# Optimization experiments

Measured on AMD Instinct MI355X. Metric: run time of the kernel, lower is better.

## Reference

```python
import jax, jax.numpy as jnp
import numpy as np

B, R, L, F, H = 65536, 12, 16, 8, 64  # batch, rss_dim, n_leds, led_feat_dim, head_dim

def setup_inputs() -> dict:
    key = jax.random.key(0)
    ks = jax.random.split(key, 20)
    p = lambda k, shp, s=0.1: (jax.random.normal(k, shp, dtype=jnp.float32) * s)
    return {
        "rss_t": jax.random.uniform(ks[0], (B, R, 1), dtype=jnp.float32),
        "led_features": jax.random.normal(ks[1], (B, L, F), dtype=jnp.float32),
        "led_positions": jax.random.normal(ks[2], (B, L, 3), dtype=jnp.float32),
        "prev_pos": jax.random.normal(ks[3], (B, 3), dtype=jnp.float32),
        "freq_mask": jax.random.randint(ks[4], (R, L), 0, 2).astype(jnp.int32),
        # intensity_gate: Linear(1,16) -> ReLU -> Linear(16,1) -> Sigmoid
        "gw1": p(ks[5], (1, 16)), "gb1": p(ks[6], (16,)),
        "gw2": p(ks[7], (16, 1)), "gb2": p(ks[8], (1,)),
        # query_proj: Linear(1,32) -> ReLU -> Linear(32,64)
        "qw1": p(ks[9], (1, 32)), "qb1": p(ks[10], (32,)),
        "qw2": p(ks[11], (32, H)), "qb2": p(ks[12], (H,)),
        # key_proj: Linear(F+3,32) -> ReLU -> Linear(32,64)
        "kw1": p(ks[13], (F + 3, 32)), "kb1": p(ks[14], (32,)),
        "kw2": p(ks[15], (32, H)), "kb2": p(ks[16], (H,)),
        "sigma": jnp.float32(0.5),
    }

def reference(rss_t, led_features, led_positions, prev_pos, freq_mask,
              gw1, gb1, gw2, gb2, qw1, qb1, qw2, qb2, kw1, kb1, kw2, kb2, sigma):
    # intensity gate with hard threshold
    gate = jax.nn.sigmoid(jax.nn.relu(rss_t @ gw1 + gb1) @ gw2 + gb2)  # [B,R,1]
    iw = (rss_t > 0.5).astype(rss_t.dtype) * gate                      # [B,R,1]
    # query / key projections
    Q = jax.nn.relu((rss_t * iw) @ qw1 + qb1) @ qw2 + qb2              # [B,R,H]
    led_input = jnp.concatenate([led_features, led_positions], axis=-1)  # [B,L,F+3]
    K = jax.nn.relu(led_input @ kw1 + kb1) @ kw2 + kb2                 # [B,L,H]
    scores = jnp.einsum("brh,blh->brl", Q, K)                          # [B,R,L]
    # distance bias
    dist_sq = jnp.sum((prev_pos[:, None, :] - led_positions) ** 2, axis=-1)  # [B,L]
    scores = scores - dist_sq[:, None, :] / (2.0 * sigma ** 2)
    # mask + softmax
    neg = jnp.finfo(scores.dtype).min
    scores = jnp.where(freq_mask[None, :, :] == 0, neg, scores)
    attn = jax.nn.softmax(scores, axis=-1)                             # [B,R,L]
    return attn, iw.squeeze(-1)
```

## Files before the change

### kernel.cpp

```cpp
#include <hip/hip_runtime.h>

#define B_TOT 65536
#define R 12
#define L 16
#define NB 16
#define NEG_MIN -3.402823466e38f

#define WS_V   0
#define WS_C   32
#define WS_PM  40
#define WS_BP  64
#define WS_TAB 96
#define TROW   72

typedef __attribute__((ext_vector_type(8))) short short8;
typedef __attribute__((ext_vector_type(4))) float f32x4;

static __device__ __forceinline__ short f2bf(float f) {
    uint32_t u = __float_as_uint(f);
    uint32_t r = u + 0x7FFFu + ((u >> 16) & 1u);
    return (short)(r >> 16);
}

__global__ __launch_bounds__(256) void nfh_pre(
    const float* __restrict__ qw1, const float* __restrict__ qb1,
    const float* __restrict__ qw2, const float* __restrict__ qb2,
    const float* __restrict__ kw2, const float* __restrict__ kb2,
    const int*   __restrict__ fmask,
    float* __restrict__ ws)
{
    __shared__ float sM[1024];
    __shared__ float su[32];
    __shared__ float sw1[32], sb1[32], sbp[32];
    const int t = threadIdx.x;

    if (t < 32) { sw1[t] = qw1[t]; sb1[t] = qb1[t]; }
    for (int e = t; e < 1024; e += 256) {
        const int i = e >> 5, j = e & 31;
        float acc = 0.f;
        for (int h = 0; h < 64; ++h) acc = fmaf(qw2[i * 64 + h], kw2[j * 64 + h], acc);
        sM[e] = acc;
    }
    if (t < 32) {
        float au = 0.f, av = 0.f;
        for (int h = 0; h < 64; ++h) {
            au = fmaf(qw2[t * 64 + h], kb2[h], au);
            av = fmaf(kw2[t * 64 + h], qb2[h], av);
        }
        su[t] = au;
        ws[WS_V + t] = av;
        const float w = qw1[t];
        sbp[t] = (w != 0.f) ? (-qb1[t] / w) : 3.0e30f;
    }
    if (t == 64) {
        float acc = 0.f;
        for (int h = 0; h < 64; ++h) acc = fmaf(qb2[h], kb2[h], acc);
        ws[WS_C] = acc;
    }
    if (t < 12) {
        int pm = 0;
        for (int l = 0; l < 16; ++l) if (fmask[t * 16 + l] != 0) pm |= (1 << l);
        ((int*)ws)[WS_PM + t] = pm;
    }
    __syncthreads();
    if (t == 0) {
        for (int i = 1; i < 32; ++i) {
            float key = sbp[i]; int j = i - 1;
            while (j >= 0 && sbp[j] > key) { sbp[j + 1] = sbp[j]; --j; }
            sbp[j + 1] = key;
        }
    }
    __syncthreads();
    if (t < 32) ws[WS_BP + t] = sbp[t];

    for (int task = t; task < 33 * 32 + 33; task += 256) {
        const int m = (task < 33 * 32) ? (task >> 5) : (task - 33 * 32);
        const float xi = (m == 0) ? sbp[0] - 1.f
                       : ((m == 32) ? sbp[31] + 1.f
                                    : sbp[m - 1] + 0.5f * (sbp[m] - sbp[m - 1]));
        if (task < 33 * 32) {
            const int j = task & 31;
            float A = 0.f, Bv = 0.f;
            for (int i = 0; i < 32; ++i) {
                if (fmaf(sw1[i], xi, sb1[i]) > 0.f) {
                    A  = fmaf(sw1[i], sM[i * 32 + j], A);
                    Bv = fmaf(sb1[i], sM[i * 32 + j], Bv);
                }
            }
            ws[WS_TAB + m * TROW + j] = A;
            ws[WS_TAB + m * TROW + 36 + j] = Bv;
        } else {
            float Au = 0.f, Bu = 0.f;
            for (int i = 0; i < 32; ++i) {
                if (fmaf(sw1[i], xi, sb1[i]) > 0.f) {
                    Au = fmaf(sw1[i], su[i], Au);
                    Bu = fmaf(sb1[i], su[i], Bu);
                }
            }
            ws[WS_TAB + m * TROW + 32] = Au;
            ws[WS_TAB + m * TROW + 36 + 32] = Bu;
        }
    }
}

__global__ __launch_bounds__(256) void nfh_main(
    const float* __restrict__ rss,
    const float* __restrict__ feat,
    const float* __restrict__ pos,
    const float* __restrict__ prev,
    const float* __restrict__ gw1, const float* __restrict__ gb1,
    const float* __restrict__ gw2, const float* __restrict__ gb2,
    const float* __restrict__ kw1, const float* __restrict__ kb1,
    const float* __restrict__ sigma_p,
    const float* __restrict__ ws,
    float* __restrict__ out)
{
    __shared__ short s_bhf[NB * 512];
    __shared__ short s_ttf[NB * 512];
    __shared__ float s_vb[NB * 16];
    __shared__ float s_tc[NB * 16];
    __shared__ int   s_pm[16];

    const int t = threadIdx.x;
    const int b0 = blockIdx.x * NB;
    const float sigma = sigma_p[0];
    const float inv2s2 = 1.f / (2.f * sigma * sigma);

    if (t < 16) s_pm[t] = (t < 12) ? ((const int*)ws)[WS_PM + t] : 0;

    {
        const int bb1 = t >> 4, l1 = t & 15;
        const int b = b0 + bb1;
        float in[11];
        const float4* f4 = (const float4*)(feat + ((size_t)b * (L * 8) + l1 * 8));
        const float4 fa = f4[0], fb = f4[1];
        in[0] = fa.x; in[1] = fa.y; in[2] = fa.z; in[3] = fa.w;
        in[4] = fb.x; in[5] = fb.y; in[6] = fb.z; in[7] = fb.w;
        const float* pp = pos + ((size_t)b * (L * 3) + l1 * 3);
        in[8] = pp[0]; in[9] = pp[1]; in[10] = pp[2];

        float dsq = 0.f;
        #pragma unroll
        for (int m = 0; m < 3; ++m) {
            const float d = prev[b * 3 + m] - in[8 + m];
            dsq = fmaf(d, d, dsq);
        }
        float bh[32];
        #pragma unroll
        for (int j = 0; j < 32; ++j) bh[j] = kb1[j];
        #pragma unroll
        for (int m = 0; m < 11; ++m) {
            const float im = in[m];
            #pragma unroll
            for (int j = 0; j < 32; ++j) bh[j] = fmaf(im, kw1[m * 32 + j], bh[j]);
        }
        float vb = ws[WS_C];
        #pragma unroll
        for (int j = 0; j < 32; ++j) {
            bh[j] = fmaxf(bh[j], 0.f);
            vb = fmaf(ws[WS_V + j], bh[j], vb);
        }
        s_vb[bb1 * 16 + l1] = vb - dsq * inv2s2;

        #pragma unroll
        for (int kb = 0; kb < 4; ++kb) {
            short8 pk;
            #pragma unroll
            for (int j = 0; j < 8; ++j) pk[j] = f2bf(bh[kb * 8 + j]);
            *(short8*)&s_bhf[bb1 * 512 + (kb * 16 + l1) * 8] = pk;
        }
    }

    if (t < NB * R) {
        const int bb2 = t / R;
        const int r2 = t - bb2 * R;
        const float x = rss[(size_t)b0 * R + t];
        float z = gb2[0];
        #pragma unroll
        for (int i = 0; i < 16; ++i) {
            const float h = fmaxf(fmaf(x, gw1[i], gb1[i]), 0.f);
            z = fmaf(h, gw2[i], z);
        }
        const float gate = 1.f / (1.f + __expf(-z));
        const float iw = (x > 0.5f) ? gate : 0.f;
        out[(size_t)B_TOT * R * L + (size_t)b0 * R + t] = iw;
        const float xq = x * iw;

        int k = 0;
        #pragma unroll
        for (int m = 0; m < 32; ++m) k += (xq > ws[WS_BP + m]) ? 1 : 0;
        const float* row = ws + WS_TAB + k * TROW;
        const float4* ra = (const float4*)row;
        const float4* rb = (const float4*)(row + 36);
        s_tc[bb2 * 16 + r2] = fmaf(xq, row[32], row[68]);
        #pragma unroll
        for (int kb = 0; kb < 4; ++kb) {
            const float4 a0 = ra[kb * 2], b0_ = rb[kb * 2];
            const float4 a1 = ra[kb * 2 + 1], b1_ = rb[kb * 2 + 1];
            short8 pk;
            pk[0] = f2bf(fmaf(xq, a0.x, b0_.x));
            pk[1] = f2bf(fmaf(xq, a0.y, b0_.y));
            pk[2] = f2bf(fmaf(xq, a0.z, b0_.z));
            pk[3] = f2bf(fmaf(xq, a0.w, b0_.w));
            pk[4] = f2bf(fmaf(xq, a1.x, b1_.x));
            pk[5] = f2bf(fmaf(xq, a1.y, b1_.y));
            pk[6] = f2bf(fmaf(xq, a1.z, b1_.z));
            pk[7] = f2bf(fmaf(xq, a1.w, b1_.w));
            *(short8*)&s_ttf[bb2 * 512 + (kb * 16 + r2) * 8] = pk;
        }
    } else {
        const int u = t - 192;
        const int bb = u >> 2, r = 12 + (u & 3);
        const short8 z8 = {0, 0, 0, 0, 0, 0, 0, 0};
        #pragma unroll
        for (int kb = 0; kb < 4; ++kb)
            *(short8*)&s_ttf[bb * 512 + (kb * 16 + r) * 8] = z8;
        s_tc[bb * 16 + r] = 0.f;
    }
    __syncthreads();

    {
        const int lane = t & 63;
        const int w = t >> 6;
        const int r = lane & 15;
        const int lg = lane >> 4;
        const int pm = s_pm[r];

        #pragma unroll
        for (int i = 0; i < 4; ++i) {
            const int bb = w * 4 + i;
            const short8 af = *(const short8*)&s_bhf[bb * 512 + lane * 8];
            const short8 bf = *(const short8*)&s_ttf[bb * 512 + lane * 8];
            f32x4 acc = {0.f, 0.f, 0.f, 0.f};
            acc = __builtin_amdgcn_mfma_f32_16x16x32_bf16(af, bf, acc, 0, 0, 0);

            const float tc = s_tc[bb * 16 + r];
            const f32x4 vb4 = *(const f32x4*)&s_vb[bb * 16 + lg * 4];

            float sc[4];
            #pragma unroll
            for (int j = 0; j < 4; ++j) {
                sc[j] = acc[j] + tc + vb4[j];
                if (!((pm >> (lg * 4 + j)) & 1)) sc[j] = NEG_MIN;
            }
            float mx = fmaxf(fmaxf(sc[0], sc[1]), fmaxf(sc[2], sc[3]));
            mx = fmaxf(mx, __shfl_xor(mx, 16));
            mx = fmaxf(mx, __shfl_xor(mx, 32));
            float sum = 0.f;
            #pragma unroll
            for (int j = 0; j < 4; ++j) { sc[j] = __expf(sc[j] - mx); sum += sc[j]; }
            sum += __shfl_xor(sum, 16);
            sum += __shfl_xor(sum, 32);
            const float inv = 1.f / sum;

            if (r < R) {
                float4* op = (float4*)(out + ((size_t)(b0 + bb) * R + r) * L + lg * 4);
                *op = make_float4(sc[0] * inv, sc[1] * inv, sc[2] * inv, sc[3] * inv);
            }
        }
    }
}

extern "C" void kernel_launch(void* const* d_in, const int* in_sizes, int n_in,
                              void* d_out, int out_size, void* d_ws, size_t ws_size,
                              hipStream_t stream) {
    const float* rss   = (const float*)d_in[0];
    const float* feat  = (const float*)d_in[1];
    const float* pos   = (const float*)d_in[2];
    const float* prev  = (const float*)d_in[3];
    const int*   fmask = (const int*)d_in[4];
    const float* gw1   = (const float*)d_in[5];
    const float* gb1   = (const float*)d_in[6];
    const float* gw2   = (const float*)d_in[7];
    const float* gb2   = (const float*)d_in[8];
    const float* qw1   = (const float*)d_in[9];
    const float* qb1   = (const float*)d_in[10];
    const float* qw2   = (const float*)d_in[11];
    const float* qb2   = (const float*)d_in[12];
    const float* kw1   = (const float*)d_in[13];
    const float* kb1   = (const float*)d_in[14];
    const float* kw2   = (const float*)d_in[15];
    const float* kb2   = (const float*)d_in[16];
    const float* sigma = (const float*)d_in[17];
    float* out = (float*)d_out;
    float* ws  = (float*)d_ws;

    nfh_pre<<<1, 256, 0, stream>>>(qw1, qb1, qw2, qb2, kw2, kb2, fmask, ws);
    nfh_main<<<B_TOT / NB, 256, 0, stream>>>(
        rss, feat, pos, prev,
        gw1, gb1, gw2, gb2, kw1, kb1,
        sigma, ws, out);
}
```

Baseline: 181.6 us.

## Compute key hidden layer with bf16 MFMA and fold value bias into query table

Replaces the per-thread scalar FMA loop for the key MLP first layer with a 32x32x16 bf16 MFMA. The inputs are features, positions and a constant 1 for the bias, packed into LDS, and the packed kw1/kb1 weights are precomputed in the pre-kernel. The v·bh + c value-bias term is folded into the query lookup table, so the main kernel no longer computes it per LED. Block size drops to 8 batches and 128 threads, and LDS strides are padded, presumably to avoid bank conflicts. This trades heavy scalar ALU work for matrix-core work, but rounding inputs to bf16 before the first layer adds precision error.

```diff
diff --git a/kernel.cpp b/kernel.cpp
--- a/kernel.cpp
+++ b/kernel.cpp
@@ -3,7 +3,7 @@
 #define B_TOT 65536
 #define R 12
 #define L 16
-#define NB 16
+#define NB 8
 #define NEG_MIN -3.402823466e38f
 
 #define WS_V   0
@@ -12,26 +12,39 @@
 #define WS_BP  64
 #define WS_TAB 96
 #define TROW   72
-
-typedef __attribute__((ext_vector_type(8))) short short8;
-typedef __attribute__((ext_vector_type(4))) float f32x4;
+#define WS_KW  2472
+
+#define TTF_BSTR 520
+#define BHF_BSTR 576
+
+typedef __attribute__((ext_vector_type(8)))  short short8;
+typedef __attribute__((ext_vector_type(4)))  float f32x4;
+typedef __attribute__((ext_vector_type(16))) float f32x16;
 
 static __device__ __forceinline__ short f2bf(float f) {
     uint32_t u = __float_as_uint(f);
     uint32_t r = u + 0x7FFFu + ((u >> 16) & 1u);
     return (short)(r >> 16);
 }
+static __device__ __forceinline__ int pack2(float f0, float f1) {
+    uint32_t u0 = __float_as_uint(f0), u1 = __float_as_uint(f1);
+    uint32_t r0 = u0 + 0x7FFFu + ((u0 >> 16) & 1u);
+    uint32_t r1 = u1 + 0x7FFFu + ((u1 >> 16) & 1u);
+    return (int)((r0 >> 16) | (r1 & 0xFFFF0000u));
+}
 
 __global__ __launch_bounds__(256) void nfh_pre(
     const float* __restrict__ qw1, const float* __restrict__ qb1,
     const float* __restrict__ qw2, const float* __restrict__ qb2,
+    const float* __restrict__ kw1, const float* __restrict__ kb1,
     const float* __restrict__ kw2, const float* __restrict__ kb2,
     const int*   __restrict__ fmask,
     float* __restrict__ ws)
 {
     __shared__ float sM[1024];
-    __shared__ float su[32];
+    __shared__ float su[32], sv[32];
     __shared__ float sw1[32], sb1[32], sbp[32];
+    __shared__ float scc[1];
     const int t = threadIdx.x;
 
     if (t < 32) { sw1[t] = qw1[t]; sb1[t] = qb1[t]; }
@@ -48,6 +61,7 @@
             av = fmaf(kw2[t * 64 + h], qb2[h], av);
         }
         su[t] = au;
+        sv[t] = av;
         ws[WS_V + t] = av;
         const float w = qw1[t];
         sbp[t] = (w != 0.f) ? (-qb1[t] / w) : 3.0e30f;
@@ -56,11 +70,26 @@
         float acc = 0.f;
         for (int h = 0; h < 64; ++h) acc = fmaf(qb2[h], kb2[h], acc);
         ws[WS_C] = acc;
+        scc[0] = acc;
     }
     if (t < 12) {
         int pm = 0;
         for (int l = 0; l < 16; ++l) if (fmask[t * 16 + l] != 0) pm |= (1 << l);
         ((int*)ws)[WS_PM + t] = pm;
+    }
+    if (t < 64) {
+        const int j = t & 31;
+        int w4[4];
+        #pragma unroll
+        for (int q = 0; q < 4; ++q) {
+            float v0, v1;
+            const int k0 = (t >> 5) * 8 + q * 2, k1 = k0 + 1;
+            v0 = (k0 < 11) ? kw1[k0 * 32 + j] : ((k0 == 11) ? kb1[j] : 0.f);
+            v1 = (k1 < 11) ? kw1[k1 * 32 + j] : ((k1 == 11) ? kb1[j] : 0.f);
+            w4[q] = pack2(v0, v1);
+        }
+        int* wp = (int*)ws + WS_KW + t * 4;
+        wp[0] = w4[0]; wp[1] = w4[1]; wp[2] = w4[2]; wp[3] = w4[3];
     }
     __syncthreads();
     if (t == 0) {
@@ -88,7 +117,7 @@
                 }
             }
             ws[WS_TAB + m * TROW + j] = A;
-            ws[WS_TAB + m * TROW + 36 + j] = Bv;
+            ws[WS_TAB + m * TROW + 36 + j] = Bv + sv[j];
         } else {
             float Au = 0.f, Bu = 0.f;
             for (int i = 0; i < 32; ++i) {
@@ -98,26 +127,26 @@
                 }
             }
             ws[WS_TAB + m * TROW + 32] = Au;
-            ws[WS_TAB + m * TROW + 36 + 32] = Bu;
-        }
-    }
-}
-
-__global__ __launch_bounds__(256) void nfh_main(
+            ws[WS_TAB + m * TROW + 36 + 32] = Bu + scc[0];
+        }
+    }
+}
+
+__global__ __launch_bounds__(128) void nfh_main(
     const float* __restrict__ rss,
     const float* __restrict__ feat,
     const float* __restrict__ pos,
     const float* __restrict__ prev,
     const float* __restrict__ gw1, const float* __restrict__ gb1,
     const float* __restrict__ gw2, const float* __restrict__ gb2,
-    const float* __restrict__ kw1, const float* __restrict__ kb1,
     const float* __restrict__ sigma_p,
     const float* __restrict__ ws,
     float* __restrict__ out)
 {
-    __shared__ short s_bhf[NB * 512];
-    __shared__ short s_ttf[NB * 512];
-    __shared__ float s_vb[NB * 16];
+    __shared__ short s_inf[(NB / 2) * 512];
+    __shared__ short s_bhf[NB * BHF_BSTR];
+    __shared__ short s_ttf[NB * TTF_BSTR];
+    __shared__ float s_dsq[NB * 16];
     __shared__ float s_tc[NB * 16];
     __shared__ int   s_pm[16];
 
@@ -129,46 +158,28 @@
     if (t < 16) s_pm[t] = (t < 12) ? ((const int*)ws)[WS_PM + t] : 0;
 
     {
-        const int bb1 = t >> 4, l1 = t & 15;
-        const int b = b0 + bb1;
-        float in[11];
-        const float4* f4 = (const float4*)(feat + ((size_t)b * (L * 8) + l1 * 8));
+        const int bb = t >> 4, l = t & 15;
+        const int b = b0 + bb;
+        const int p = bb >> 1, m = (bb & 1) * 16 + l;
+        const float4* f4 = (const float4*)(feat + ((size_t)b * (L * 8) + l * 8));
         const float4 fa = f4[0], fb = f4[1];
-        in[0] = fa.x; in[1] = fa.y; in[2] = fa.z; in[3] = fa.w;
-        in[4] = fb.x; in[5] = fb.y; in[6] = fb.z; in[7] = fb.w;
-        const float* pp = pos + ((size_t)b * (L * 3) + l1 * 3);
-        in[8] = pp[0]; in[9] = pp[1]; in[10] = pp[2];
+        const float* pp = pos + ((size_t)b * (L * 3) + l * 3);
+        const float p0 = pp[0], p1 = pp[1], p2 = pp[2];
 
         float dsq = 0.f;
-        #pragma unroll
-        for (int m = 0; m < 3; ++m) {
-            const float d = prev[b * 3 + m] - in[8 + m];
-            dsq = fmaf(d, d, dsq);
-        }
-        float bh[32];
-        #pragma unroll
-        for (int j = 0; j < 32; ++j) bh[j] = kb1[j];
-        #pragma unroll
-        for (int m = 0; m < 11; ++m) {
-            const float im = in[m];
-            #pragma unroll
-            for (int j = 0; j < 32; ++j) bh[j] = fmaf(im, kw1[m * 32 + j], bh[j]);
-        }
-        float vb = ws[WS_C];
-        #pragma unroll
-        for (int j = 0; j < 32; ++j) {
-            bh[j] = fmaxf(bh[j], 0.f);
-            vb = fmaf(ws[WS_V + j], bh[j], vb);
-        }
-        s_vb[bb1 * 16 + l1] = vb - dsq * inv2s2;
-
-        #pragma unroll
-        for (int kb = 0; kb < 4; ++kb) {
-            short8 pk;
-            #pragma unroll
-            for (int j = 0; j < 8; ++j) pk[j] = f2bf(bh[kb * 8 + j]);
-            *(short8*)&s_bhf[bb1 * 512 + (kb * 16 + l1) * 8] = pk;
-        }
+        {
+            float d0 = prev[b * 3 + 0] - p0, d1 = prev[b * 3 + 1] - p1, d2 = prev[b * 3 + 2] - p2;
+            dsq = fmaf(d0, d0, fmaf(d1, d1, d2 * d2));
+        }
+        s_dsq[bb * 16 + l] = -dsq * inv2s2;
+
+        int4 w0, w1;
+        w0.x = pack2(fa.x, fa.y); w0.y = pack2(fa.z, fa.w);
+        w0.z = pack2(fb.x, fb.y); w0.w = pack2(fb.z, fb.w);
+        w1.x = pack2(p0, p1);     w1.y = pack2(p2, 1.0f);
+        w1.z = 0;                 w1.w = 0;
+        *(int4*)&s_inf[p * 512 + m * 8]        = w0;
+        *(int4*)&s_inf[p * 512 + (32 + m) * 8] = w1;
     }
 
     if (t < NB * R) {
@@ -197,25 +208,45 @@
         for (int kb = 0; kb < 4; ++kb) {
             const float4 a0 = ra[kb * 2], b0_ = rb[kb * 2];
             const float4 a1 = ra[kb * 2 + 1], b1_ = rb[kb * 2 + 1];
-            short8 pk;
-            pk[0] = f2bf(fmaf(xq, a0.x, b0_.x));
-            pk[1] = f2bf(fmaf(xq, a0.y, b0_.y));
-            pk[2] = f2bf(fmaf(xq, a0.z, b0_.z));
-            pk[3] = f2bf(fmaf(xq, a0.w, b0_.w));
-            pk[4] = f2bf(fmaf(xq, a1.x, b1_.x));
-            pk[5] = f2bf(fmaf(xq, a1.y, b1_.y));
-            pk[6] = f2bf(fmaf(xq, a1.z, b1_.z));
-            pk[7] = f2bf(fmaf(xq, a1.w, b1_.w));
-            *(short8*)&s_ttf[bb2 * 512 + (kb * 16 + r2) * 8] = pk;
+            int4 pk;
+            pk.x = pack2(fmaf(xq, a0.x, b0_.x), fmaf(xq, a0.y, b0_.y));
+            pk.y = pack2(fmaf(xq, a0.z, b0_.z), fmaf(xq, a0.w, b0_.w));
+            pk.z = pack2(fmaf(xq, a1.x, b1_.x), fmaf(xq, a1.y, b1_.y));
+            pk.w = pack2(fmaf(xq, a1.z, b1_.z), fmaf(xq, a1.w, b1_.w));
+            *(int4*)&s_ttf[bb2 * TTF_BSTR + (kb * 16 + r2) * 8] = pk;
         }
     } else {
-        const int u = t - 192;
+        const int u = t - 96;
         const int bb = u >> 2, r = 12 + (u & 3);
-        const short8 z8 = {0, 0, 0, 0, 0, 0, 0, 0};
+        const int4 z4 = {0, 0, 0, 0};
         #pragma unroll
         for (int kb = 0; kb < 4; ++kb)
-            *(short8*)&s_ttf[bb * 512 + (kb * 16 + r) * 8] = z8;
+            *(int4*)&s_ttf[bb * TTF_BSTR + (kb * 16 + r) * 8] = z4;
         s_tc[bb * 16 + r] = 0.f;
+    }
+    __syncthreads();
+
+    {
+        const int lane = t & 63;
+        const int w = t >> 6;
+        const int j = lane & 31;
+        const int jk = (j >> 3) * 136 + (j & 7);
+        const short8 bfk = *(const short8*)((const int*)ws + WS_KW + lane * 4);
+
+        #pragma unroll
+        for (int pp = 0; pp < 2; ++pp) {
+            const int p = w * 2 + pp;
+            const short8 af = *(const short8*)&s_inf[p * 512 + lane * 8];
+            f32x16 acc = {0.f,0.f,0.f,0.f,0.f,0.f,0.f,0.f,0.f,0.f,0.f,0.f,0.f,0.f,0.f,0.f};
+            acc = __builtin_amdgcn_mfma_f32_32x32x16_bf16(af, bfk, acc, 0, 0, 0);
+            #pragma unroll
+            for (int rg = 0; rg < 16; ++rg) {
+                const int rrow = (rg & 3) + 8 * (rg >> 2) + 4 * (lane >> 5);
+                const int l = rrow & 15;
+                const int bb = p * 2 + (rrow >> 4);
+                s_bhf[bb * BHF_BSTR + l * 8 + jk] = f2bf(fmaxf(acc[rg], 0.f));
+            }
+        }
     }
     __syncthreads();
 
@@ -225,30 +256,32 @@
         const int r = lane & 15;
         const int lg = lane >> 4;
         const int pm = s_pm[r];
+        const int aoff = lg * 272 + (lane & 15) * 8;
+        const int a_sh = (lane >> 4) * 136 + (lane & 15) * 8;
 
         #pragma unroll
         for (int i = 0; i < 4; ++i) {
             const int bb = w * 4 + i;
-            const short8 af = *(const short8*)&s_bhf[bb * 512 + lane * 8];
-            const short8 bf = *(const short8*)&s_ttf[bb * 512 + lane * 8];
+            const short8 af = *(const short8*)&s_bhf[bb * BHF_BSTR + a_sh];
+            const short8 bf = *(const short8*)&s_ttf[bb * TTF_BSTR + lane * 8];
             f32x4 acc = {0.f, 0.f, 0.f, 0.f};
             acc = __builtin_amdgcn_mfma_f32_16x16x32_bf16(af, bf, acc, 0, 0, 0);
 
             const float tc = s_tc[bb * 16 + r];
-            const f32x4 vb4 = *(const f32x4*)&s_vb[bb * 16 + lg * 4];
+            const f32x4 d4 = *(const f32x4*)&s_dsq[bb * 16 + lg * 4];
 
             float sc[4];
             #pragma unroll
-            for (int j = 0; j < 4; ++j) {
-                sc[j] = acc[j] + tc + vb4[j];
-                if (!((pm >> (lg * 4 + j)) & 1)) sc[j] = NEG_MIN;
+            for (int jj = 0; jj < 4; ++jj) {
+                sc[jj] = acc[jj] + tc + d4[jj];
+                if (!((pm >> (lg * 4 + jj)) & 1)) sc[jj] = NEG_MIN;
             }
             float mx = fmaxf(fmaxf(sc[0], sc[1]), fmaxf(sc[2], sc[3]));
             mx = fmaxf(mx, __shfl_xor(mx, 16));
             mx = fmaxf(mx, __shfl_xor(mx, 32));
             float sum = 0.f;
             #pragma unroll
-            for (int j = 0; j < 4; ++j) { sc[j] = __expf(sc[j] - mx); sum += sc[j]; }
+            for (int jj = 0; jj < 4; ++jj) { sc[jj] = __expf(sc[jj] - mx); sum += sc[jj]; }
             sum += __shfl_xor(sum, 16);
             sum += __shfl_xor(sum, 32);
             const float inv = 1.f / sum;
@@ -258,6 +291,7 @@
                 *op = make_float4(sc[0] * inv, sc[1] * inv, sc[2] * inv, sc[3] * inv);
             }
         }
+        (void)aoff;
     }
 }
 
@@ -285,9 +319,9 @@
     float* out = (float*)d_out;
     float* ws  = (float*)d_ws;
 
-    nfh_pre<<<1, 256, 0, stream>>>(qw1, qb1, qw2, qb2, kw2, kb2, fmask, ws);
-    nfh_main<<<B_TOT / NB, 256, 0, stream>>>(
+    nfh_pre<<<1, 256, 0, stream>>>(qw1, qb1, qw2, qb2, kw1, kb1, kw2, kb2, fmask, ws);
+    nfh_main<<<B_TOT / NB, 128, 0, stream>>>(
         rss, feat, pos, prev,
-        gw1, gb1, gw2, gb2, kw1, kb1,
+        gw1, gb1, gw2, gb2,
         sigma, ws, out);
 }
```

Result: no change. 184.4 us (+1.6%).
